# Kernel optimization log

Measured on AMD Instinct MI355X. Metric: run time of the kernel, lower is better.

Reference implementation:

```python
import jax, jax.numpy as jnp
import numpy as np

B, T, D, H, L = 128, 1024, 64, 256, 2


def setup_inputs() -> dict:
    key = jax.random.key(0)
    ks = jax.random.split(key, 18)
    s = 1.0 / np.sqrt(H)

    def u(k, shape):
        return jax.random.uniform(k, shape, jnp.float32, -s, s)

    inp = {
        "x": jax.random.normal(ks[0], (B, T, D), jnp.float32),
        "lengths": jax.random.randint(ks[1], (B,), T // 2, T + 1).at[0].set(T),
        "tf_mask": jax.random.uniform(ks[2], (T,)) < 0.5,
    }
    # encoder LSTM params (torch gate order i,f,g,o; biases b_ih+b_hh fused)
    inp["enc_Wih0"] = u(ks[3], (4 * H, D)); inp["enc_Whh0"] = u(ks[4], (4 * H, H)); inp["enc_b0"] = u(ks[5], (4 * H,))
    inp["enc_Wih1"] = u(ks[6], (4 * H, H)); inp["enc_Whh1"] = u(ks[7], (4 * H, H)); inp["enc_b1"] = u(ks[8], (4 * H,))
    # decoder LSTM params
    inp["dec_Wih0"] = u(ks[9], (4 * H, D)); inp["dec_Whh0"] = u(ks[10], (4 * H, H)); inp["dec_b0"] = u(ks[11], (4 * H,))
    inp["dec_Wih1"] = u(ks[12], (4 * H, H)); inp["dec_Whh1"] = u(ks[13], (4 * H, H)); inp["dec_b1"] = u(ks[14], (4 * H,))
    # output projection hidden_dim -> input_dim
    inp["out_W"] = u(ks[15], (D, H)); inp["out_b"] = u(ks[16], (D,))
    return inp


def lstm_cell(x, h, c, Wih, Whh, b):
    z = x @ Wih.T + h @ Whh.T + b  # [B, 4H]
    i, f, g, o = jnp.split(z, 4, axis=-1)
    c_new = jax.nn.sigmoid(f) * c + jax.nn.sigmoid(i) * jnp.tanh(g)
    h_new = jax.nn.sigmoid(o) * jnp.tanh(c_new)
    return h_new, c_new


def reference(x, lengths, tf_mask, enc_Wih0, enc_Whh0, enc_b0, enc_Wih1, enc_Whh1, enc_b1,
              dec_Wih0, dec_Whh0, dec_b0, dec_Wih1, dec_Whh1, dec_b1, out_W, out_b):
    enc_p = ((enc_Wih0, enc_Whh0, enc_b0), (enc_Wih1, enc_Whh1, enc_b1))
    dec_p = ((dec_Wih0, dec_Whh0, dec_b0), (dec_Wih1, dec_Whh1, dec_b1))
    b, t = x.shape[0], x.shape[1]
    xt_seq = jnp.swapaxes(x, 0, 1)  # [T, B, D]
    h0 = jnp.zeros((L, b, H), x.dtype)
    c0 = jnp.zeros((L, b, H), x.dtype)

    # --- encoder: packed-sequence semantics via validity masking ---
    def enc_step(carry, inp):
        h, c = carry
        xt, step = inp
        valid = (step < lengths)[:, None]  # [B,1]
        a = xt
        hs, cs = [], []
        for l in range(L):
            hn, cn = lstm_cell(a, h[l], c[l], *enc_p[l])
            hn = jnp.where(valid, hn, h[l])  # freeze state past length
            cn = jnp.where(valid, cn, c[l])
            hs.append(hn); cs.append(cn); a = hn
        out = jnp.where(valid, hs[-1], jnp.zeros_like(hs[-1]))  # pad with zeros
        return (jnp.stack(hs), jnp.stack(cs)), out

    (hT, cT), enc_outs = jax.lax.scan(enc_step, (h0, c0), (xt_seq, jnp.arange(t)))
    encoder_out = jnp.swapaxes(enc_outs, 0, 1)  # [B, T, H]

    # --- decoder: per-step LSTM + projection + teacher forcing ---
    def dec_step(carry, inp):
        h, c, dec_in = carry
        xt, tf = inp
        a = dec_in
        hs, cs = [], []
        for l in range(L):
            hn, cn = lstm_cell(a, h[l], c[l], *dec_p[l])
            hs.append(hn); cs.append(cn); a = hn
        out = a @ out_W.T + out_b  # [B, D]
        nxt = jnp.where(tf, xt, out)
        return (jnp.stack(hs), jnp.stack(cs), nxt), out

    _, dec_outs = jax.lax.scan(dec_step, (hT, cT, x[:, -1, :]), (xt_seq, tf_mask))
    outputs = jnp.swapaxes(dec_outs, 0, 1)  # [B, T, D]
    return outputs, encoder_out
```

## Files before the change

### kernel.cpp

```cpp
#include <hip/hip_runtime.h>
#include <cstdint>
#include <cstddef>


typedef _Float16 f16x8 __attribute__((ext_vector_type(8)));
typedef float    f32x4 __attribute__((ext_vector_type(4)));
typedef unsigned int u32x4 __attribute__((ext_vector_type(4)));

#define AROWS 608

constexpr size_t OFF_E0  = 0;
constexpr size_t OFF_E1  = 655360;
constexpr size_t OFF_D0  = 1703936;
constexpr size_t OFF_D1  = 2359296;
constexpr size_t OFF_OW  = 3407872;
constexpr size_t OFF_H0  = 3440640;
constexpr size_t OFF_H1  = 3702784;
constexpr size_t OFF_XH  = 3964928;

__device__ __forceinline__ void st_coh128(void* p, u32x4 v){
  asm volatile("global_store_dwordx4 %0, %1, off sc0 sc1"
               :: "v"((unsigned long long)(uintptr_t)p), "v"(v) : "memory");
}
__device__ __forceinline__ void ldg2_coh(const void* p0, const void* p1, u32x4& a, u32x4& b){
  asm volatile("global_load_dwordx4 %0, %2, off sc0 sc1\n\t"
               "global_load_dwordx4 %1, %3, off sc0 sc1\n\t"
               "s_waitcnt vmcnt(0)"
               : "=&v"(a), "=&v"(b)
               : "v"((unsigned long long)(uintptr_t)p0),
                 "v"((unsigned long long)(uintptr_t)p1) : "memory");
}
__device__ __forceinline__ void ldg4_coh(const void* p0, const void* p1, const void* p2, const void* p3,
                                         u32x4& a, u32x4& b, u32x4& c, u32x4& d){
  asm volatile("global_load_dwordx4 %0, %4, off sc0 sc1\n\t"
               "global_load_dwordx4 %1, %5, off sc0 sc1\n\t"
               "global_load_dwordx4 %2, %6, off sc0 sc1\n\t"
               "global_load_dwordx4 %3, %7, off sc0 sc1\n\t"
               "s_waitcnt vmcnt(0)"
               : "=&v"(a), "=&v"(b), "=&v"(c), "=&v"(d)
               : "v"((unsigned long long)(uintptr_t)p0),
                 "v"((unsigned long long)(uintptr_t)p1),
                 "v"((unsigned long long)(uintptr_t)p2),
                 "v"((unsigned long long)(uintptr_t)p3) : "memory");
}

__device__ __forceinline__ void poll2(const void* p0, const void* p1,
                                      u32x4& a, u32x4& b, int& dead){
  if(dead) return;
  for(int gu = 0;; ++gu){
    ldg2_coh(p0, p1, a, b);
    unsigned bad = 0;
#pragma unroll
    for(int j = 0; j < 4; ++j) bad |= (a[j]==0xFFFFFFFFu) | (b[j]==0xFFFFFFFFu);
    if(!bad) return;
    if(gu > 60000){ dead = 1; return; }
  }
}

__device__ __forceinline__ float sigm(float z){ return 1.f/(1.f + __expf(-z)); }
__device__ __forceinline__ float tanh_(float z){ return 2.f/(1.f + __expf(-2.f*z)) - 1.f; }

template<int KS>
__device__ __forceinline__ f32x4 gemm_tile(const _Float16* A, int am, int q, const f16x8* wf){
  f32x4 a0 = {0.f,0.f,0.f,0.f}, a1 = {0.f,0.f,0.f,0.f};
#pragma unroll
  for(int ks = 0; ks < KS; ++ks){
    f16x8 av = *(const f16x8*)(A + am*AROWS + ks*32 + q*8);
    if(ks & 1) a1 = __builtin_amdgcn_mfma_f32_16x16x32_f16(av, wf[ks], a1, 0, 0, 0);
    else       a0 = __builtin_amdgcn_mfma_f32_16x16x32_f16(av, wf[ks], a0, 0, 0, 0);
  }
  return a0 + a1;
}

__global__ void lstm_xcvt(const float* __restrict__ xin, _Float16* __restrict__ xh){
  size_t i = ((size_t)blockIdx.x * 256 + threadIdx.x) * 8;
  float4 a = *(const float4*)(xin + i);
  float4 b = *(const float4*)(xin + i + 4);
  union { _Float16 h[8]; u32x4 v; } o;
  o.h[0]=(_Float16)a.x; o.h[1]=(_Float16)a.y; o.h[2]=(_Float16)a.z; o.h[3]=(_Float16)a.w;
  o.h[4]=(_Float16)b.x; o.h[5]=(_Float16)b.y; o.h[6]=(_Float16)b.z; o.h[7]=(_Float16)b.w;
  *(u32x4*)(xh + i) = o.v;
}

__global__ void lstm_packw(const float* eW0, const float* eU0, const float* eW1, const float* eU1,
                           const float* dW0, const float* dU0, const float* dW1, const float* dU1,
                           const float* oW, char* ws){
  int c = blockIdx.x * 256 + threadIdx.x;
  const float *Wih, *Whh; _Float16* dst; int KS, Kin, cc;
  if(c < 40960)      { Wih=eW0; Whh=eU0; dst=(_Float16*)(ws+OFF_E0); KS=10; Kin=64;  cc=c; }
  else if(c < 106496){ Wih=eW1; Whh=eU1; dst=(_Float16*)(ws+OFF_E1); KS=16; Kin=256; cc=c-40960; }
  else if(c < 147456){ Wih=dW0; Whh=dU0; dst=(_Float16*)(ws+OFF_D0); KS=10; Kin=64;  cc=c-106496; }
  else if(c < 212992){ Wih=dW1; Whh=dU1; dst=(_Float16*)(ws+OFF_D1); KS=16; Kin=256; cc=c-147456; }
  else{
    cc = c - 212992;
    int l = cc & 63, t1 = cc >> 6, ks = t1 & 7, nt = t1 >> 3;
    int n = nt*16 + (l & 15), kb = ks*32 + ((l >> 4) << 3);
    union { _Float16 h[8]; u32x4 v; } o;
#pragma unroll
    for(int j = 0; j < 8; ++j) o.h[j] = (_Float16)oW[n*256 + kb + j];
    *(u32x4*)((_Float16*)(ws + OFF_OW) + (size_t)cc*8) = o.v;
    return;
  }
  int l = cc & 63, t1 = cc >> 6, ks, t2;
  if(KS == 10){ ks = t1 % 10; t2 = t1 / 10; } else { ks = t1 & 15; t2 = t1 >> 4; }
  int rr = t2 & 15, wg = t2 >> 4;
  int row = wg*256 + rr*16 + (l & 15);
  int kb  = ks*32 + ((l >> 4) << 3);
  union { _Float16 h[8]; u32x4 v; } o;
#pragma unroll
  for(int j = 0; j < 8; ++j){
    int k = kb + j;
    float s = (k < Kin) ? Wih[row*Kin + k] : Whh[row*256 + (k - Kin)];
    o.h[j] = (_Float16)s;
  }
  *(u32x4*)(dst + (size_t)cc*8) = o.v;
}

__global__ __launch_bounds__(256, 1)
void lstm_persist(const float* __restrict__ x, const int* __restrict__ lengths,
                  const int* __restrict__ tf,
                  const float* __restrict__ eb0, const float* __restrict__ eb1,
                  const float* __restrict__ db0, const float* __restrict__ db1,
                  const float* __restrict__ outb,
                  float* __restrict__ dout, char* __restrict__ ws)
{
  const int tid = threadIdx.x;
  const int lane = tid & 63, w = tid >> 6;
  const int g = blockIdx.x >> 4, r = blockIdx.x & 15;
  const int gb = g * 16;
  const int tb = tid >> 4, th = tid & 15;
  const int am = lane & 15, q = lane >> 4;
  const int m0 = tid >> 5, kc = tid & 31;
  const int hco = (kc >> 1)*256 + (kc & 1)*8 + m0*16 + g*4096;
  const int slice = g*4096 + r*256;

  _Float16* Xh    = (_Float16*)(ws + OFF_XH);
  _Float16* h0buf = (_Float16*)(ws + OFF_H0);
  _Float16* h1buf = (_Float16*)(ws + OFF_H1);
  float* outD = dout;
  float* outE = dout + (size_t)128*1024*64;

  __shared__ alignas(16) _Float16 Abuf[16*AROWS];
  __shared__ float zbuf[4][16][17];
  __shared__ alignas(16) _Float16 dinbuf[16][80];
  __shared__ alignas(16) _Float16 hsh[256];

  float c0 = 0.f, c1 = 0.f, h0p = 0.f, h1p = 0.f;
  const int len_b = lengths[gb + tb];
  int dead = 0;
  const u32x4 PZ = {0xFFFFFFFFu,0xFFFFFFFFu,0xFFFFFFFFu,0xFFFFFFFFu};

  u32x4 H0ra, H0rb;
  u32x4 H1ca, H1cb;

  float be0[4], be1[4];
#pragma unroll
  for(int j = 0; j < 4; ++j){
    be0[j] = eb0[j*256 + r*16 + th];
    be1[j] = eb1[j*256 + r*16 + th];
  }

  f16x8 wf0[10], wf1[16], wfo[8];
  {
    const f16x8* p0 = (const f16x8*)(ws + OFF_E0);
    const f16x8* p1 = (const f16x8*)(ws + OFF_E1);
#pragma unroll
    for(int ks = 0; ks < 10; ++ks) wf0[ks] = p0[((w*16 + r)*10 + ks)*64 + lane];
#pragma unroll
    for(int ks = 0; ks < 16; ++ks) wf1[ks] = p1[((w*16 + r)*16 + ks)*64 + lane];
  }

  for(int t = 0; t <= 1024; ++t){
    const int sh0 = (t+3)&3;
    const int sh1 = (t+2)&3;
    u32x4 a, b, H1a, H1b;
    const _Float16 *h1q0, *h1q1;

    if(t < 1024 && tid < 128){
      int mm = tid >> 3, k0 = (tid & 7) * 8;
      *(f16x8*)(Abuf + mm*AROWS + k0) =
          *(const f16x8*)(Xh + ((size_t)(gb + mm)*1024 + t)*64 + k0);
    }
    {
      const _Float16* b0 = h0buf + sh0*32768 + hco;
      const _Float16* b1 = b0 + 128;
      h1q0 = h1buf + sh1*32768 + hco;
      h1q1 = h1q0 + 128;
      ldg4_coh(b0, b1, h1q0, h1q1, a, b, H1a, H1b);
      unsigned bad = 0;
#pragma unroll
      for(int j = 0; j < 4; ++j) bad |= (a[j]==0xFFFFFFFFu) | (b[j]==0xFFFFFFFFu);
      if(bad) poll2(b0, b1, a, b, dead);
      *(f16x8*)(Abuf + m0*AROWS + 64 + kc*8)     = __builtin_bit_cast(f16x8, a);
      *(f16x8*)(Abuf + (m0+8)*AROWS + 64 + kc*8) = __builtin_bit_cast(f16x8, b);
      H0ra = a; H0rb = b;
    }
    __syncthreads();

    if(t < 1024){
      {
        f32x4 z = gemm_tile<10>(Abuf, am, q, wf0);
#pragma unroll
        for(int i = 0; i < 4; ++i) zbuf[w][q*4 + i][am] = z[i];
      }
      __syncthreads();
      {
        float zi = zbuf[0][tb][th] + be0[0];
        float zf = zbuf[1][tb][th] + be0[1];
        float zg = zbuf[2][tb][th] + be0[2];
        float zo = zbuf[3][tb][th] + be0[3];
        float cn = sigm(zf)*c0 + sigm(zi)*tanh_(zg);
        float hn = sigm(zo)*tanh_(cn);
        bool valid = t < len_b;
        c0  = valid ? cn : c0;
        h0p = valid ? hn : h0p;
        hsh[tb*16 + th] = (_Float16)h0p;
      }
      __syncthreads();
      if(tid < 32)
        st_coh128(h0buf + (t&3)*32768 + slice + tid*8, *(const u32x4*)&hsh[tid*8]);
    }

    if(t >= 1){
      unsigned bad = 0;
#pragma unroll
      for(int j = 0; j < 4; ++j) bad |= (H1a[j]==0xFFFFFFFFu) | (H1b[j]==0xFFFFFFFFu);
      if(bad) poll2(h1q0, h1q1, H1a, H1b, dead);
      *(f16x8*)(Abuf + m0*AROWS + 320 + kc*8)     = __builtin_bit_cast(f16x8, H1a);
      *(f16x8*)(Abuf + (m0+8)*AROWS + 320 + kc*8) = __builtin_bit_cast(f16x8, H1b);
      if(tid < 64){
        _Float16* basep = (tid < 32) ? (h0buf + ((t+2)&3)*32768)
                                     : (h1buf + ((t+1)&3)*32768);
        st_coh128(basep + slice + (tid&31)*8, PZ);
      }
      __syncthreads();

      {
        f32x4 z = gemm_tile<16>(Abuf + 64, am, q, wf1);
#pragma unroll
        for(int i = 0; i < 4; ++i) zbuf[w][q*4 + i][am] = z[i];
      }
      __syncthreads();
      {
        const int u = t - 1;
        float zi = zbuf[0][tb][th] + be1[0];
        float zf = zbuf[1][tb][th] + be1[1];
        float zg = zbuf[2][tb][th] + be1[2];
        float zo = zbuf[3][tb][th] + be1[3];
        float cn = sigm(zf)*c1 + sigm(zi)*tanh_(zg);
        float hn = sigm(zo)*tanh_(cn);
        bool valid = u < len_b;
        c1  = valid ? cn : c1;
        h1p = valid ? hn : h1p;
        outE[((size_t)(gb + tb)*1024 + u)*256 + r*16 + th] = valid ? h1p : 0.f;
        hsh[tb*16 + th] = (_Float16)h1p;
      }
      __syncthreads();
      if(tid < 32)
        st_coh128(h1buf + ((t+3)&3)*32768 + slice + tid*8, *(const u32x4*)&hsh[tid*8]);
    }
  }

  {
    const f16x8* p0 = (const f16x8*)(ws + OFF_D0);
    const f16x8* p1 = (const f16x8*)(ws + OFF_D1);
    const f16x8* po = (const f16x8*)(ws + OFF_OW);
#pragma unroll
    for(int ks = 0; ks < 10; ++ks) wf0[ks] = p0[((w*16 + r)*10 + ks)*64 + lane];
#pragma unroll
    for(int ks = 0; ks < 16; ++ks) wf1[ks] = p1[((w*16 + r)*16 + ks)*64 + lane];
#pragma unroll
    for(int ks = 0; ks < 8;  ++ks) wfo[ks] = po[(w*8 + ks)*64 + lane];
  }
  float bd0[4], bd1[4], ob[4];
#pragma unroll
  for(int j = 0; j < 4; ++j){
    bd0[j] = db0[j*256 + r*16 + th];
    bd1[j] = db1[j*256 + r*16 + th];
    ob[j]  = outb[th*4 + j];
  }
  {
    float4 xv = *(const float4*)(x + ((size_t)(gb + tb)*1024 + 1023)*64 + th*4);
    dinbuf[tb][th*4 + 0] = (_Float16)xv.x;
    dinbuf[tb][th*4 + 1] = (_Float16)xv.y;
    dinbuf[tb][th*4 + 2] = (_Float16)xv.z;
    dinbuf[tb][th*4 + 3] = (_Float16)xv.w;
  }
  __syncthreads();

  {
    const _Float16* b0 = h1buf + 3*32768 + hco;
    const _Float16* b1 = b0 + 128;
    ldg2_coh(b0, b1, H1ca, H1cb);
    unsigned bad = 0;
#pragma unroll
    for(int j = 0; j < 4; ++j) bad |= (H1ca[j]==0xFFFFFFFFu) | (H1cb[j]==0xFFFFFFFFu);
    if(bad) poll2(b0, b1, H1ca, H1cb, dead);
  }
  if(tid < 32)
    st_coh128(h1buf + 2*32768 + slice + tid*8, PZ);

  for(int d = 0; d < 1024; ++d){
    const int s4 = d & 3;

    if(tid < 128){
      int mm = tid >> 3, k0 = (tid & 7) * 8;
      *(f16x8*)(Abuf + mm*AROWS + k0) = *(const f16x8*)(&dinbuf[mm][k0]);
    }
    *(f16x8*)(Abuf + m0*AROWS + 64 + kc*8)     = __builtin_bit_cast(f16x8, H0ra);
    *(f16x8*)(Abuf + (m0+8)*AROWS + 64 + kc*8) = __builtin_bit_cast(f16x8, H0rb);
    __syncthreads();

    {
      f32x4 z = gemm_tile<10>(Abuf, am, q, wf0);
#pragma unroll
      for(int i = 0; i < 4; ++i) zbuf[w][q*4 + i][am] = z[i];
    }
    __syncthreads();
    {
      float zi = zbuf[0][tb][th] + bd0[0];
      float zf = zbuf[1][tb][th] + bd0[1];
      float zg = zbuf[2][tb][th] + bd0[2];
      float zo = zbuf[3][tb][th] + bd0[3];
      float cn = sigm(zf)*c0 + sigm(zi)*tanh_(zg);
      float hn = sigm(zo)*tanh_(cn);
      c0 = cn;
      hsh[tb*16 + th] = (_Float16)hn;
    }
    __syncthreads();
    if(tid < 32)
      st_coh128(h0buf + s4*32768 + slice + tid*8, *(const u32x4*)&hsh[tid*8]);

    *(f16x8*)(Abuf + m0*AROWS + 256 + kc*8)     = __builtin_bit_cast(f16x8, H1ca);
    *(f16x8*)(Abuf + (m0+8)*AROWS + 256 + kc*8) = __builtin_bit_cast(f16x8, H1cb);
    {
      const _Float16* b0 = h0buf + s4*32768 + hco;
      const _Float16* b1 = b0 + 128;
      u32x4 a, b;
      ldg2_coh(b0, b1, a, b);
      unsigned bad = 0;
#pragma unroll
      for(int j = 0; j < 4; ++j) bad |= (a[j]==0xFFFFFFFFu) | (b[j]==0xFFFFFFFFu);
      if(bad) poll2(b0, b1, a, b, dead);
      *(f16x8*)(Abuf + m0*AROWS + kc*8)       = __builtin_bit_cast(f16x8, a);
      *(f16x8*)(Abuf + (m0+8)*AROWS + kc*8)   = __builtin_bit_cast(f16x8, b);
      H0ra = a; H0rb = b;
    }
    if(tid < 64){
      _Float16* basep = ((tid < 32) ? h0buf : h1buf) + ((d+3)&3)*32768;
      st_coh128(basep + slice + (tid&31)*8, PZ);
    }
    __syncthreads();

    {
      f32x4 z = gemm_tile<16>(Abuf, am, q, wf1);
#pragma unroll
      for(int i = 0; i < 4; ++i) zbuf[w][q*4 + i][am] = z[i];
    }
    __syncthreads();
    {
      float zi = zbuf[0][tb][th] + bd1[0];
      float zf = zbuf[1][tb][th] + bd1[1];
      float zg = zbuf[2][tb][th] + bd1[2];
      float zo = zbuf[3][tb][th] + bd1[3];
      float cn = sigm(zf)*c1 + sigm(zi)*tanh_(zg);
      float hn = sigm(zo)*tanh_(cn);
      c1 = cn;
      hsh[tb*16 + th] = (_Float16)hn;
    }
    __syncthreads();
    if(tid < 32)
      st_coh128(h1buf + s4*32768 + slice + tid*8, *(const u32x4*)&hsh[tid*8]);

    {
      const _Float16* b0 = h1buf + s4*32768 + hco;
      const _Float16* b1 = b0 + 128;
      ldg2_coh(b0, b1, H1ca, H1cb);
      unsigned bad = 0;
#pragma unroll
      for(int j = 0; j < 4; ++j) bad |= (H1ca[j]==0xFFFFFFFFu) | (H1cb[j]==0xFFFFFFFFu);
      if(bad) poll2(b0, b1, H1ca, H1cb, dead);
      *(f16x8*)(Abuf + m0*AROWS + kc*8)     = __builtin_bit_cast(f16x8, H1ca);
      *(f16x8*)(Abuf + (m0+8)*AROWS + kc*8) = __builtin_bit_cast(f16x8, H1cb);
    }
    __syncthreads();

    {
      f32x4 z = gemm_tile<8>(Abuf, am, q, wfo);
#pragma unroll
      for(int i = 0; i < 4; ++i) zbuf[w][q*4 + i][am] = z[i];
    }
    __syncthreads();

    {
      float o[4];
#pragma unroll
      for(int i = 0; i < 4; ++i)
        o[i] = zbuf[th >> 2][tb][(th & 3)*4 + i] + ob[i];
      if(r == 0){
        float4 v; v.x = o[0]; v.y = o[1]; v.z = o[2]; v.w = o[3];
        *(float4*)(outD + ((size_t)(gb + tb)*1024 + d)*64 + th*4) = v;
      }
      if(tf[d] != 0){
        float4 xv = *(const float4*)(x + ((size_t)(gb + tb)*1024 + d)*64 + th*4);
        o[0] = xv.x; o[1] = xv.y; o[2] = xv.z; o[3] = xv.w;
      }
#pragma unroll
      for(int i = 0; i < 4; ++i) dinbuf[tb][th*4 + i] = (_Float16)o[i];
    }
    __syncthreads();
  }
}

extern "C" void kernel_launch(void* const* d_in, const int* in_sizes, int n_in,
                              void* d_out, int out_size, void* d_ws, size_t ws_size,
                              hipStream_t stream){
  const float* x   = (const float*)d_in[0];
  const int* lens  = (const int*)d_in[1];
  const int* tfm   = (const int*)d_in[2];
  const float* eW0 = (const float*)d_in[3];
  const float* eU0 = (const float*)d_in[4];
  const float* eb0 = (const float*)d_in[5];
  const float* eW1 = (const float*)d_in[6];
  const float* eU1 = (const float*)d_in[7];
  const float* eb1 = (const float*)d_in[8];
  const float* dW0 = (const float*)d_in[9];
  const float* dU0 = (const float*)d_in[10];
  const float* db0 = (const float*)d_in[11];
  const float* dW1 = (const float*)d_in[12];
  const float* dU1 = (const float*)d_in[13];
  const float* db1 = (const float*)d_in[14];
  const float* oW  = (const float*)d_in[15];
  const float* ob  = (const float*)d_in[16];
  char* ws = (char*)d_ws;

  hipMemsetAsync(ws + OFF_H0,            0xFF, 3*65536, stream);
  hipMemsetAsync(ws + OFF_H0 + 3*65536,  0x00, 65536,   stream);
  hipMemsetAsync(ws + OFF_H1,            0xFF, 3*65536, stream);
  hipMemsetAsync(ws + OFF_H1 + 3*65536,  0x00, 65536,   stream);
  lstm_xcvt <<<dim3(4096), dim3(256), 0, stream>>>(x, (_Float16*)(ws + OFF_XH));
  lstm_packw<<<dim3(840),  dim3(256), 0, stream>>>(eW0, eU0, eW1, eU1,
                                                   dW0, dU0, dW1, dU1, oW, ws);
  lstm_persist<<<dim3(128), dim3(256), 0, stream>>>(x, lens, tfm, eb0, eb1,
                                                    db0, db1, ob,
                                                    (float*)d_out, ws);
}
```

Measured before the change: 7.565 ms.

## Map batch groups to XCDs and use L2-local coherence for exchanges

```diff
diff --git a/kernel.cpp b/kernel.cpp
--- a/kernel.cpp
+++ b/kernel.cpp
@@ -17,44 +17,101 @@
 constexpr size_t OFF_H0  = 3440640;
 constexpr size_t OFF_H1  = 3702784;
 constexpr size_t OFF_XH  = 3964928;
-
+constexpr size_t OFF_TBL = 20742144;
+
+__device__ __forceinline__ void l1_inv(){
+  asm volatile("buffer_inv sc0" ::: "memory");
+}
+
+template<int MODE>
+__device__ __forceinline__ void ldg2_m(const void* p0, const void* p1, u32x4& a, u32x4& b){
+  if constexpr(MODE == 0)
+    asm volatile("global_load_dwordx4 %0, %2, off sc0\n\t"
+                 "global_load_dwordx4 %1, %3, off sc0\n\t"
+                 "s_waitcnt vmcnt(0)"
+                 : "=&v"(a), "=&v"(b)
+                 : "v"((unsigned long long)(uintptr_t)p0),
+                   "v"((unsigned long long)(uintptr_t)p1) : "memory");
+  else
+    asm volatile("global_load_dwordx4 %0, %2, off sc0 sc1\n\t"
+                 "global_load_dwordx4 %1, %3, off sc0 sc1\n\t"
+                 "s_waitcnt vmcnt(0)"
+                 : "=&v"(a), "=&v"(b)
+                 : "v"((unsigned long long)(uintptr_t)p0),
+                   "v"((unsigned long long)(uintptr_t)p1) : "memory");
+}
+template<int MODE>
+__device__ __forceinline__ void ldg4_m(const void* p0, const void* p1, const void* p2, const void* p3,
+                                       u32x4& a, u32x4& b, u32x4& c, u32x4& d){
+  if constexpr(MODE == 0)
+    asm volatile("global_load_dwordx4 %0, %4, off sc0\n\t"
+                 "global_load_dwordx4 %1, %5, off sc0\n\t"
+                 "global_load_dwordx4 %2, %6, off sc0\n\t"
+                 "global_load_dwordx4 %3, %7, off sc0\n\t"
+                 "s_waitcnt vmcnt(0)"
+                 : "=&v"(a), "=&v"(b), "=&v"(c), "=&v"(d)
+                 : "v"((unsigned long long)(uintptr_t)p0),
+                   "v"((unsigned long long)(uintptr_t)p1),
+                   "v"((unsigned long long)(uintptr_t)p2),
+                   "v"((unsigned long long)(uintptr_t)p3) : "memory");
+  else
+    asm volatile("global_load_dwordx4 %0, %4, off sc0 sc1\n\t"
+                 "global_load_dwordx4 %1, %5, off sc0 sc1\n\t"
+                 "global_load_dwordx4 %2, %6, off sc0 sc1\n\t"
+                 "global_load_dwordx4 %3, %7, off sc0 sc1\n\t"
+                 "s_waitcnt vmcnt(0)"
+                 : "=&v"(a), "=&v"(b), "=&v"(c), "=&v"(d)
+                 : "v"((unsigned long long)(uintptr_t)p0),
+                   "v"((unsigned long long)(uintptr_t)p1),
+                   "v"((unsigned long long)(uintptr_t)p2),
+                   "v"((unsigned long long)(uintptr_t)p3) : "memory");
+}
+
+template<bool LOCAL>
 __device__ __forceinline__ void st_coh128(void* p, u32x4 v){
   asm volatile("global_store_dwordx4 %0, %1, off sc0 sc1"
                :: "v"((unsigned long long)(uintptr_t)p), "v"(v) : "memory");
-}
+  if constexpr(LOCAL)
+    asm volatile("global_store_dwordx4 %0, %1, off sc0"
+                 :: "v"((unsigned long long)(uintptr_t)p), "v"(v) : "memory");
+}
+
+template<bool LOCAL>
 __device__ __forceinline__ void ldg2_coh(const void* p0, const void* p1, u32x4& a, u32x4& b){
-  asm volatile("global_load_dwordx4 %0, %2, off sc0 sc1\n\t"
-               "global_load_dwordx4 %1, %3, off sc0 sc1\n\t"
-               "s_waitcnt vmcnt(0)"
-               : "=&v"(a), "=&v"(b)
-               : "v"((unsigned long long)(uintptr_t)p0),
-                 "v"((unsigned long long)(uintptr_t)p1) : "memory");
-}
+  if constexpr(LOCAL){ l1_inv(); ldg2_m<0>(p0, p1, a, b); }
+  else ldg2_m<1>(p0, p1, a, b);
+}
+template<bool LOCAL>
 __device__ __forceinline__ void ldg4_coh(const void* p0, const void* p1, const void* p2, const void* p3,
                                          u32x4& a, u32x4& b, u32x4& c, u32x4& d){
-  asm volatile("global_load_dwordx4 %0, %4, off sc0 sc1\n\t"
-               "global_load_dwordx4 %1, %5, off sc0 sc1\n\t"
-               "global_load_dwordx4 %2, %6, off sc0 sc1\n\t"
-               "global_load_dwordx4 %3, %7, off sc0 sc1\n\t"
-               "s_waitcnt vmcnt(0)"
-               : "=&v"(a), "=&v"(b), "=&v"(c), "=&v"(d)
-               : "v"((unsigned long long)(uintptr_t)p0),
-                 "v"((unsigned long long)(uintptr_t)p1),
-                 "v"((unsigned long long)(uintptr_t)p2),
-                 "v"((unsigned long long)(uintptr_t)p3) : "memory");
-}
-
+  if constexpr(LOCAL){ l1_inv(); ldg4_m<0>(p0, p1, p2, p3, a, b, c, d); }
+  else ldg4_m<1>(p0, p1, p2, p3, a, b, c, d);
+}
+
+template<bool LOCAL>
 __device__ __forceinline__ void poll2(const void* p0, const void* p1,
                                       u32x4& a, u32x4& b, int& dead){
   if(dead) return;
   for(int gu = 0;; ++gu){
-    ldg2_coh(p0, p1, a, b);
+    if(LOCAL && gu < 6){ l1_inv(); ldg2_m<0>(p0, p1, a, b); }
+    else ldg2_m<1>(p0, p1, a, b);
     unsigned bad = 0;
 #pragma unroll
     for(int j = 0; j < 4; ++j) bad |= (a[j]==0xFFFFFFFFu) | (b[j]==0xFFFFFFFFu);
     if(!bad) return;
     if(gu > 60000){ dead = 1; return; }
   }
+}
+
+__device__ __forceinline__ int ldg_sys_i32(const int* p){
+  int v;
+  asm volatile("global_load_dword %0, %1, off sc0 sc1\n\ts_waitcnt vmcnt(0)"
+               : "=v"(v) : "v"((unsigned long long)(uintptr_t)p) : "memory");
+  return v;
+}
+__device__ __forceinline__ void stg_sys_i32(int* p, int v){
+  asm volatile("global_store_dword %0, %1, off sc0 sc1"
+               :: "v"((unsigned long long)(uintptr_t)p), "v"(v) : "memory");
 }
 
 __device__ __forceinline__ float sigm(float z){ return 1.f/(1.f + __expf(-z)); }
@@ -116,17 +173,25 @@
   *(u32x4*)(dst + (size_t)cc*8) = o.v;
 }
 
-__global__ __launch_bounds__(256, 1)
-void lstm_persist(const float* __restrict__ x, const int* __restrict__ lengths,
-                  const int* __restrict__ tf,
-                  const float* __restrict__ eb0, const float* __restrict__ eb1,
-                  const float* __restrict__ db0, const float* __restrict__ db1,
-                  const float* __restrict__ outb,
-                  float* __restrict__ dout, char* __restrict__ ws)
+struct Shm {
+  alignas(16) _Float16 Abuf[16*AROWS];
+  float zbuf[4][16][17];
+  alignas(16) _Float16 dinbuf[16][80];
+  alignas(16) _Float16 hsh[256];
+};
+
+template<bool LOCAL>
+__device__ __forceinline__ void core(
+    const float* __restrict__ x, const int* __restrict__ lengths,
+    const int* __restrict__ tf,
+    const float* __restrict__ eb0, const float* __restrict__ eb1,
+    const float* __restrict__ db0, const float* __restrict__ db1,
+    const float* __restrict__ outb,
+    float* __restrict__ dout, char* __restrict__ ws,
+    const int g, const int r, Shm* sh)
 {
   const int tid = threadIdx.x;
   const int lane = tid & 63, w = tid >> 6;
-  const int g = blockIdx.x >> 4, r = blockIdx.x & 15;
   const int gb = g * 16;
   const int tb = tid >> 4, th = tid & 15;
   const int am = lane & 15, q = lane >> 4;
@@ -140,10 +205,10 @@
   float* outD = dout;
   float* outE = dout + (size_t)128*1024*64;
 
-  __shared__ alignas(16) _Float16 Abuf[16*AROWS];
-  __shared__ float zbuf[4][16][17];
-  __shared__ alignas(16) _Float16 dinbuf[16][80];
-  __shared__ alignas(16) _Float16 hsh[256];
+  _Float16* Abuf = sh->Abuf;
+  auto& zbuf   = sh->zbuf;
+  auto& dinbuf = sh->dinbuf;
+  _Float16* hsh = sh->hsh;
 
   float c0 = 0.f, c1 = 0.f, h0p = 0.f, h1p = 0.f;
   const int len_b = lengths[gb + tb];
@@ -186,11 +251,11 @@
       const _Float16* b1 = b0 + 128;
       h1q0 = h1buf + sh1*32768 + hco;
       h1q1 = h1q0 + 128;
-      ldg4_coh(b0, b1, h1q0, h1q1, a, b, H1a, H1b);
+      ldg4_coh<LOCAL>(b0, b1, h1q0, h1q1, a, b, H1a, H1b);
       unsigned bad = 0;
 #pragma unroll
       for(int j = 0; j < 4; ++j) bad |= (a[j]==0xFFFFFFFFu) | (b[j]==0xFFFFFFFFu);
-      if(bad) poll2(b0, b1, a, b, dead);
+      if(bad) poll2<LOCAL>(b0, b1, a, b, dead);
       *(f16x8*)(Abuf + m0*AROWS + 64 + kc*8)     = __builtin_bit_cast(f16x8, a);
       *(f16x8*)(Abuf + (m0+8)*AROWS + 64 + kc*8) = __builtin_bit_cast(f16x8, b);
       H0ra = a; H0rb = b;
@@ -218,20 +283,20 @@
       }
       __syncthreads();
       if(tid < 32)
-        st_coh128(h0buf + (t&3)*32768 + slice + tid*8, *(const u32x4*)&hsh[tid*8]);
+        st_coh128<LOCAL>(h0buf + (t&3)*32768 + slice + tid*8, *(const u32x4*)&hsh[tid*8]);
     }
 
     if(t >= 1){
       unsigned bad = 0;
 #pragma unroll
       for(int j = 0; j < 4; ++j) bad |= (H1a[j]==0xFFFFFFFFu) | (H1b[j]==0xFFFFFFFFu);
-      if(bad) poll2(h1q0, h1q1, H1a, H1b, dead);
+      if(bad) poll2<LOCAL>(h1q0, h1q1, H1a, H1b, dead);
       *(f16x8*)(Abuf + m0*AROWS + 320 + kc*8)     = __builtin_bit_cast(f16x8, H1a);
       *(f16x8*)(Abuf + (m0+8)*AROWS + 320 + kc*8) = __builtin_bit_cast(f16x8, H1b);
       if(tid < 64){
         _Float16* basep = (tid < 32) ? (h0buf + ((t+2)&3)*32768)
                                      : (h1buf + ((t+1)&3)*32768);
-        st_coh128(basep + slice + (tid&31)*8, PZ);
+        st_coh128<LOCAL>(basep + slice + (tid&31)*8, PZ);
       }
       __syncthreads();
 
@@ -257,7 +322,7 @@
       }
       __syncthreads();
       if(tid < 32)
-        st_coh128(h1buf + ((t+3)&3)*32768 + slice + tid*8, *(const u32x4*)&hsh[tid*8]);
+        st_coh128<LOCAL>(h1buf + ((t+3)&3)*32768 + slice + tid*8, *(const u32x4*)&hsh[tid*8]);
     }
   }
 
@@ -291,14 +356,14 @@
   {
     const _Float16* b0 = h1buf + 3*32768 + hco;
     const _Float16* b1 = b0 + 128;
-    ldg2_coh(b0, b1, H1ca, H1cb);
+    ldg2_coh<LOCAL>(b0, b1, H1ca, H1cb);
     unsigned bad = 0;
 #pragma unroll
     for(int j = 0; j < 4; ++j) bad |= (H1ca[j]==0xFFFFFFFFu) | (H1cb[j]==0xFFFFFFFFu);
-    if(bad) poll2(b0, b1, H1ca, H1cb, dead);
+    if(bad) poll2<LOCAL>(b0, b1, H1ca, H1cb, dead);
   }
   if(tid < 32)
-    st_coh128(h1buf + 2*32768 + slice + tid*8, PZ);
+    st_coh128<LOCAL>(h1buf + 2*32768 + slice + tid*8, PZ);
 
   for(int d = 0; d < 1024; ++d){
     const int s4 = d & 3;
@@ -329,7 +394,7 @@
     }
     __syncthreads();
     if(tid < 32)
-      st_coh128(h0buf + s4*32768 + slice + tid*8, *(const u32x4*)&hsh[tid*8]);
+      st_coh128<LOCAL>(h0buf + s4*32768 + slice + tid*8, *(const u32x4*)&hsh[tid*8]);
 
     *(f16x8*)(Abuf + m0*AROWS + 256 + kc*8)     = __builtin_bit_cast(f16x8, H1ca);
     *(f16x8*)(Abuf + (m0+8)*AROWS + 256 + kc*8) = __builtin_bit_cast(f16x8, H1cb);
@@ -337,18 +402,18 @@
       const _Float16* b0 = h0buf + s4*32768 + hco;
       const _Float16* b1 = b0 + 128;
       u32x4 a, b;
-      ldg2_coh(b0, b1, a, b);
+      ldg2_coh<LOCAL>(b0, b1, a, b);
       unsigned bad = 0;
 #pragma unroll
       for(int j = 0; j < 4; ++j) bad |= (a[j]==0xFFFFFFFFu) | (b[j]==0xFFFFFFFFu);
-      if(bad) poll2(b0, b1, a, b, dead);
+      if(bad) poll2<LOCAL>(b0, b1, a, b, dead);
       *(f16x8*)(Abuf + m0*AROWS + kc*8)       = __builtin_bit_cast(f16x8, a);
       *(f16x8*)(Abuf + (m0+8)*AROWS + kc*8)   = __builtin_bit_cast(f16x8, b);
       H0ra = a; H0rb = b;
     }
     if(tid < 64){
       _Float16* basep = ((tid < 32) ? h0buf : h1buf) + ((d+3)&3)*32768;
-      st_coh128(basep + slice + (tid&31)*8, PZ);
+      st_coh128<LOCAL>(basep + slice + (tid&31)*8, PZ);
     }
     __syncthreads();
 
@@ -370,16 +435,16 @@
     }
     __syncthreads();
     if(tid < 32)
-      st_coh128(h1buf + s4*32768 + slice + tid*8, *(const u32x4*)&hsh[tid*8]);
+      st_coh128<LOCAL>(h1buf + s4*32768 + slice + tid*8, *(const u32x4*)&hsh[tid*8]);
 
     {
       const _Float16* b0 = h1buf + s4*32768 + hco;
       const _Float16* b1 = b0 + 128;
-      ldg2_coh(b0, b1, H1ca, H1cb);
+      ldg2_coh<LOCAL>(b0, b1, H1ca, H1cb);
       unsigned bad = 0;
 #pragma unroll
       for(int j = 0; j < 4; ++j) bad |= (H1ca[j]==0xFFFFFFFFu) | (H1cb[j]==0xFFFFFFFFu);
-      if(bad) poll2(b0, b1, H1ca, H1cb, dead);
+      if(bad) poll2<LOCAL>(b0, b1, H1ca, H1cb, dead);
       *(f16x8*)(Abuf + m0*AROWS + kc*8)     = __builtin_bit_cast(f16x8, H1ca);
       *(f16x8*)(Abuf + (m0+8)*AROWS + kc*8) = __builtin_bit_cast(f16x8, H1cb);
     }
@@ -397,7 +462,7 @@
 #pragma unroll
       for(int i = 0; i < 4; ++i)
         o[i] = zbuf[th >> 2][tb][(th & 3)*4 + i] + ob[i];
-      if(r == 0){
+      if(tb == r){
         float4 v; v.x = o[0]; v.y = o[1]; v.z = o[2]; v.w = o[3];
         *(float4*)(outD + ((size_t)(gb + tb)*1024 + d)*64 + th*4) = v;
       }
@@ -410,6 +475,61 @@
     }
     __syncthreads();
   }
+}
+
+__global__ __launch_bounds__(256, 1)
+void lstm_persist(const float* __restrict__ x, const int* __restrict__ lengths,
+                  const int* __restrict__ tf,
+                  const float* __restrict__ eb0, const float* __restrict__ eb1,
+                  const float* __restrict__ db0, const float* __restrict__ db1,
+                  const float* __restrict__ outb,
+                  float* __restrict__ dout, char* __restrict__ ws)
+{
+  const int tid = threadIdx.x;
+  __shared__ Shm sh;
+  __shared__ int s_g, s_r, s_loc;
+
+  {
+    int* tbl = (int*)(ws + OFF_TBL);
+    int xcd;
+    asm volatile("s_getreg_b32 %0, hwreg(HW_REG_XCC_ID)" : "=s"(xcd));
+    if(tid == 0) stg_sys_i32(tbl + blockIdx.x, (xcd & 7) + 1);
+    int* stbl = (int*)&sh.zbuf[0][0][0];
+    if(tid < 128){
+      int v = -1;
+      for(int it = 0; it < 2000000; ++it){
+        v = ldg_sys_i32(tbl + tid);
+        if(v != -1) break;
+      }
+      stbl[tid] = v;
+    }
+    __syncthreads();
+    if(tid == 0){
+      int cnt[8] = {0,0,0,0,0,0,0,0};
+      signed char gA[128], rA[128];
+      for(int b = 0; b < 128; ++b){
+        int xb = (stbl[b] - 1) & 7;
+        if(cnt[xb] < 16){ gA[b] = (signed char)xb; rA[b] = (signed char)cnt[xb]++; }
+        else gA[b] = -1;
+      }
+      int locmask = 0;
+      for(int xx = 0; xx < 8; ++xx) if(cnt[xx] == 16) locmask |= (1 << xx);
+      int dg = 0;
+      for(int b = 0; b < 128; ++b) if(gA[b] < 0){
+        while(cnt[dg] >= 16) ++dg;
+        gA[b] = (signed char)dg; rA[b] = (signed char)cnt[dg]++;
+      }
+      int me = blockIdx.x;
+      s_g = gA[me]; s_r = rA[me];
+      s_loc = (locmask >> gA[me]) & 1;
+    }
+    __syncthreads();
+  }
+  const int g = s_g, r = s_r, loc = s_loc;
+  __syncthreads();
+
+  if(loc) core<true >(x, lengths, tf, eb0, eb1, db0, db1, outb, dout, ws, g, r, &sh);
+  else    core<false>(x, lengths, tf, eb0, eb1, db0, db1, outb, dout, ws, g, r, &sh);
 }
 
 extern "C" void kernel_launch(void* const* d_in, const int* in_sizes, int n_in,
@@ -438,6 +558,7 @@
   hipMemsetAsync(ws + OFF_H0 + 3*65536,  0x00, 65536,   stream);
   hipMemsetAsync(ws + OFF_H1,            0xFF, 3*65536, stream);
   hipMemsetAsync(ws + OFF_H1 + 3*65536,  0x00, 65536,   stream);
+  hipMemsetAsync(ws + OFF_TBL,           0xFF, 512,     stream);
   lstm_xcvt <<<dim3(4096), dim3(256), 0, stream>>>(x, (_Float16*)(ws + OFF_XH));
   lstm_packw<<<dim3(840),  dim3(256), 0, stream>>>(eW0, eU0, eW1, eU1,
                                                    dW0, dU0, dW1, dU1, oW, ws);
```

Measured after the change: 10.78 ms. 1.42x slower.

## Defer output projection off the critical path on teacher-forced decoder steps

Applied to the files above, without the earlier changes.

```diff
diff --git a/kernel.cpp b/kernel.cpp
--- a/kernel.cpp
+++ b/kernel.cpp
@@ -42,6 +42,17 @@
                  "v"((unsigned long long)(uintptr_t)p1),
                  "v"((unsigned long long)(uintptr_t)p2),
                  "v"((unsigned long long)(uintptr_t)p3) : "memory");
+}
+__device__ __forceinline__ void ldg2_issue(const void* p0, const void* p1, u32x4& a, u32x4& b){
+  asm volatile("global_load_dwordx4 %0, %2, off sc0 sc1\n\t"
+               "global_load_dwordx4 %1, %3, off sc0 sc1"
+               : "=&v"(a), "=&v"(b)
+               : "v"((unsigned long long)(uintptr_t)p0),
+                 "v"((unsigned long long)(uintptr_t)p1) : "memory");
+}
+__device__ __forceinline__ void vm_wait0(){
+  asm volatile("s_waitcnt vmcnt(0)" ::: "memory");
+  __builtin_amdgcn_sched_barrier(0);
 }
 
 __device__ __forceinline__ void poll2(const void* p0, const void* p1,
@@ -142,6 +153,7 @@
 
   __shared__ alignas(16) _Float16 Abuf[16*AROWS];
   __shared__ float zbuf[4][16][17];
+  __shared__ float zbuf2[4][16][17];
   __shared__ alignas(16) _Float16 dinbuf[16][80];
   __shared__ alignas(16) _Float16 hsh[256];
 
@@ -279,30 +291,23 @@
     bd1[j] = db1[j*256 + r*16 + th];
     ob[j]  = outb[th*4 + j];
   }
-  {
-    float4 xv = *(const float4*)(x + ((size_t)(gb + tb)*1024 + 1023)*64 + th*4);
-    dinbuf[tb][th*4 + 0] = (_Float16)xv.x;
-    dinbuf[tb][th*4 + 1] = (_Float16)xv.y;
-    dinbuf[tb][th*4 + 2] = (_Float16)xv.z;
-    dinbuf[tb][th*4 + 3] = (_Float16)xv.w;
+  if(tid < 128){
+    int mm = tid >> 3, k0 = (tid & 7) * 8;
+    *(f16x8*)(&dinbuf[mm][k0]) =
+        *(const f16x8*)(Xh + ((size_t)(gb + mm)*1024 + 1023)*64 + k0);
   }
   __syncthreads();
 
-  {
-    const _Float16* b0 = h1buf + 3*32768 + hco;
-    const _Float16* b1 = b0 + 128;
-    ldg2_coh(b0, b1, H1ca, H1cb);
-    unsigned bad = 0;
-#pragma unroll
-    for(int j = 0; j < 4; ++j) bad |= (H1ca[j]==0xFFFFFFFFu) | (H1cb[j]==0xFFFFFFFFu);
-    if(bad) poll2(b0, b1, H1ca, H1cb, dead);
-  }
-  if(tid < 32)
-    st_coh128(h1buf + 2*32768 + slice + tid*8, PZ);
-
+  int tfprev = 0;
   for(int d = 0; d < 1024; ++d){
     const int s4 = d & 3;
-
+    const int Pdef = (d == 0) | tfprev;
+    const int Pout = (d > 0) & tfprev;
+    u32x4 Pa, Pb;
+    const _Float16* pq0 = h1buf + ((d+3)&3)*32768 + hco;
+    const _Float16* pq1 = pq0 + 128;
+
+    if(Pdef) ldg2_issue(pq0, pq1, Pa, Pb);
     if(tid < 128){
       int mm = tid >> 3, k0 = (tid & 7) * 8;
       *(f16x8*)(Abuf + mm*AROWS + k0) = *(const f16x8*)(&dinbuf[mm][k0]);
@@ -317,6 +322,17 @@
       for(int i = 0; i < 4; ++i) zbuf[w][q*4 + i][am] = z[i];
     }
     __syncthreads();
+
+    if(Pdef){
+      vm_wait0();
+      unsigned bad = 0;
+#pragma unroll
+      for(int j = 0; j < 4; ++j) bad |= (Pa[j]==0xFFFFFFFFu) | (Pb[j]==0xFFFFFFFFu);
+      if(bad) poll2(pq0, pq1, Pa, Pb, dead);
+      H1ca = Pa; H1cb = Pb;
+      if(d == 0 && tid < 32)
+        st_coh128(h1buf + 2*32768 + slice + tid*8, PZ);
+    }
     {
       float zi = zbuf[0][tb][th] + bd0[0];
       float zf = zbuf[1][tb][th] + bd0[1];
@@ -328,9 +344,9 @@
       hsh[tb*16 + th] = (_Float16)hn;
     }
     __syncthreads();
+
     if(tid < 32)
       st_coh128(h0buf + s4*32768 + slice + tid*8, *(const u32x4*)&hsh[tid*8]);
-
     *(f16x8*)(Abuf + m0*AROWS + 256 + kc*8)     = __builtin_bit_cast(f16x8, H1ca);
     *(f16x8*)(Abuf + (m0+8)*AROWS + 256 + kc*8) = __builtin_bit_cast(f16x8, H1cb);
     {
@@ -352,12 +368,26 @@
     }
     __syncthreads();
 
+    if(Pout){
+      f32x4 z = gemm_tile<8>(Abuf + 256, am, q, wfo);
+#pragma unroll
+      for(int i = 0; i < 4; ++i) zbuf2[w][q*4 + i][am] = z[i];
+    }
     {
       f32x4 z = gemm_tile<16>(Abuf, am, q, wf1);
 #pragma unroll
       for(int i = 0; i < 4; ++i) zbuf[w][q*4 + i][am] = z[i];
     }
     __syncthreads();
+
+    if(Pout && tb == r){
+      float4 v;
+      v.x = zbuf2[th >> 2][tb][(th & 3)*4 + 0] + ob[0];
+      v.y = zbuf2[th >> 2][tb][(th & 3)*4 + 1] + ob[1];
+      v.z = zbuf2[th >> 2][tb][(th & 3)*4 + 2] + ob[2];
+      v.w = zbuf2[th >> 2][tb][(th & 3)*4 + 3] + ob[3];
+      *(float4*)(outD + ((size_t)(gb + tb)*1024 + (d-1))*64 + th*4) = v;
+    }
     {
       float zi = zbuf[0][tb][th] + bd1[0];
       float zf = zbuf[1][tb][th] + bd1[1];
@@ -369,10 +399,17 @@
       hsh[tb*16 + th] = (_Float16)hn;
     }
     __syncthreads();
+
     if(tid < 32)
       st_coh128(h1buf + s4*32768 + slice + tid*8, *(const u32x4*)&hsh[tid*8]);
-
-    {
+    const int tfcur = tf[d];
+    if(tfcur != 0){
+      if(tid < 128){
+        int mm = tid >> 3, k0 = (tid & 7) * 8;
+        *(f16x8*)(&dinbuf[mm][k0]) =
+            *(const f16x8*)(Xh + ((size_t)(gb + mm)*1024 + d)*64 + k0);
+      }
+    } else {
       const _Float16* b0 = h1buf + s4*32768 + hco;
       const _Float16* b1 = b0 + 128;
       ldg2_coh(b0, b1, H1ca, H1cb);
@@ -382,33 +419,56 @@
       if(bad) poll2(b0, b1, H1ca, H1cb, dead);
       *(f16x8*)(Abuf + m0*AROWS + kc*8)     = __builtin_bit_cast(f16x8, H1ca);
       *(f16x8*)(Abuf + (m0+8)*AROWS + kc*8) = __builtin_bit_cast(f16x8, H1cb);
-    }
-    __syncthreads();
-
+      __syncthreads();
+      {
+        f32x4 z = gemm_tile<8>(Abuf, am, q, wfo);
+#pragma unroll
+        for(int i = 0; i < 4; ++i) zbuf[w][q*4 + i][am] = z[i];
+      }
+      __syncthreads();
+      {
+        float o[4];
+#pragma unroll
+        for(int i = 0; i < 4; ++i)
+          o[i] = zbuf[th >> 2][tb][(th & 3)*4 + i] + ob[i];
+        if(tb == r){
+          float4 v; v.x = o[0]; v.y = o[1]; v.z = o[2]; v.w = o[3];
+          *(float4*)(outD + ((size_t)(gb + tb)*1024 + d)*64 + th*4) = v;
+        }
+#pragma unroll
+        for(int i = 0; i < 4; ++i) dinbuf[tb][th*4 + i] = (_Float16)o[i];
+      }
+    }
+    __syncthreads();
+    tfprev = tfcur;
+  }
+
+  if(tfprev != 0){
+    const _Float16* b0 = h1buf + 3*32768 + hco;
+    const _Float16* b1 = b0 + 128;
+    u32x4 a, b;
+    ldg2_coh(b0, b1, a, b);
+    unsigned bad = 0;
+#pragma unroll
+    for(int j = 0; j < 4; ++j) bad |= (a[j]==0xFFFFFFFFu) | (b[j]==0xFFFFFFFFu);
+    if(bad) poll2(b0, b1, a, b, dead);
+    *(f16x8*)(Abuf + m0*AROWS + kc*8)     = __builtin_bit_cast(f16x8, a);
+    *(f16x8*)(Abuf + (m0+8)*AROWS + kc*8) = __builtin_bit_cast(f16x8, b);
+    __syncthreads();
     {
       f32x4 z = gemm_tile<8>(Abuf, am, q, wfo);
 #pragma unroll
       for(int i = 0; i < 4; ++i) zbuf[w][q*4 + i][am] = z[i];
     }
     __syncthreads();
-
-    {
-      float o[4];
-#pragma unroll
-      for(int i = 0; i < 4; ++i)
-        o[i] = zbuf[th >> 2][tb][(th & 3)*4 + i] + ob[i];
-      if(r == 0){
-        float4 v; v.x = o[0]; v.y = o[1]; v.z = o[2]; v.w = o[3];
-        *(float4*)(outD + ((size_t)(gb + tb)*1024 + d)*64 + th*4) = v;
-      }
-      if(tf[d] != 0){
-        float4 xv = *(const float4*)(x + ((size_t)(gb + tb)*1024 + d)*64 + th*4);
-        o[0] = xv.x; o[1] = xv.y; o[2] = xv.z; o[3] = xv.w;
-      }
-#pragma unroll
-      for(int i = 0; i < 4; ++i) dinbuf[tb][th*4 + i] = (_Float16)o[i];
-    }
-    __syncthreads();
+    if(tb == r){
+      float4 v;
+      v.x = zbuf[th >> 2][tb][(th & 3)*4 + 0] + ob[0];
+      v.y = zbuf[th >> 2][tb][(th & 3)*4 + 1] + ob[1];
+      v.z = zbuf[th >> 2][tb][(th & 3)*4 + 2] + ob[2];
+      v.w = zbuf[th >> 2][tb][(th & 3)*4 + 3] + ob[3];
+      *(float4*)(outD + ((size_t)(gb + tb)*1024 + 1023)*64 + th*4) = v;
+    }
   }
 }
 
```

After: 6.531 ms. 1.16x faster.
